# Performance work log

Measured on AMD Instinct MI355X. Metric: run time of the kernel, lower is better.

## Reference

```python
import jax, jax.numpy as jnp
import numpy as np

HIDDEN = 2048
N_HEADS = 32
N_KV = 8
HEAD_DIM = HIDDEN // N_HEADS  # 64
GROUP = N_HEADS // N_KV       # 4
FFN = 8192
EPS = 1e-5
ROPE_BASE = 500000.0
NEG = -1e9


def rms_norm(x, w, eps=EPS):
    var = jnp.mean(x * x, axis=-1, keepdims=True)
    return x * jax.lax.rsqrt(var + eps) * w


def rope_cos_sin(position_ids):
    # inv_freq: [head_dim//2]
    inv_freq = 1.0 / (ROPE_BASE ** (jnp.arange(0, HEAD_DIM, 2, dtype=jnp.float32) / HEAD_DIM))
    freqs = position_ids.astype(jnp.float32)[:, :, None] * inv_freq[None, None, :]  # [b,s,d/2]
    emb = jnp.concatenate([freqs, freqs], axis=-1)  # [b,s,d]
    return jnp.cos(emb), jnp.sin(emb)


def rotate_half(x):
    x1, x2 = jnp.split(x, 2, axis=-1)
    return jnp.concatenate([-x2, x1], axis=-1)


def setup_inputs() -> dict:
    key = jax.random.key(0)
    ks = jax.random.split(key, 12)
    b, s = 2, 1024
    scale_h = 1.0 / np.sqrt(HIDDEN)
    scale_f = 1.0 / np.sqrt(FFN)
    hidden_states = jax.random.normal(ks[0], (b, s, HIDDEN), jnp.float32)
    causal = jnp.where(jnp.tril(jnp.ones((s, s), bool)), 0.0, NEG).astype(jnp.float32)
    attention_mask = jnp.broadcast_to(causal[None, None], (b, 1, s, s))
    position_ids = jnp.broadcast_to(jnp.arange(s, dtype=jnp.int32)[None], (b, s))
    return {
        "hidden_states": hidden_states,
        "attention_mask": attention_mask,
        "wq": jax.random.normal(ks[1], (HIDDEN, N_HEADS * HEAD_DIM), jnp.float32) * scale_h,
        "wk": jax.random.normal(ks[2], (HIDDEN, N_KV * HEAD_DIM), jnp.float32) * scale_h,
        "wv": jax.random.normal(ks[3], (HIDDEN, N_KV * HEAD_DIM), jnp.float32) * scale_h,
        "wo": jax.random.normal(ks[4], (N_HEADS * HEAD_DIM, HIDDEN), jnp.float32) * scale_h,
        "norm1_w": jnp.ones((HIDDEN,), jnp.float32),
        "norm2_w": jnp.ones((HIDDEN,), jnp.float32),
        "w_gate": jax.random.normal(ks[5], (HIDDEN, FFN), jnp.float32) * scale_h,
        "w_up": jax.random.normal(ks[6], (HIDDEN, FFN), jnp.float32) * scale_h,
        "w_down": jax.random.normal(ks[7], (FFN, HIDDEN), jnp.float32) * scale_f,
        "position_ids": position_ids,
    }


def reference(hidden_states, attention_mask, wq, wk, wv, wo, norm1_w, norm2_w,
              w_gate, w_up, w_down, position_ids):
    b, s, _ = hidden_states.shape
    residual = hidden_states
    normed = rms_norm(hidden_states, norm1_w)

    q = (normed @ wq).reshape(b, s, N_HEADS, HEAD_DIM).transpose(0, 2, 1, 3)  # [b,H,s,d]
    k = (normed @ wk).reshape(b, s, N_KV, HEAD_DIM).transpose(0, 2, 1, 3)    # [b,G,s,d]
    v = (normed @ wv).reshape(b, s, N_KV, HEAD_DIM).transpose(0, 2, 1, 3)

    cos, sin = rope_cos_sin(position_ids)  # [b,s,d]
    cos, sin = cos[:, None], sin[:, None]  # unsqueeze head dim
    q = q * cos + rotate_half(q) * sin
    k = k * cos + rotate_half(k) * sin

    # repeat_kv: [b,G,s,d] -> [b,H,s,d]
    k = jnp.repeat(k, GROUP, axis=1)
    v = jnp.repeat(v, GROUP, axis=1)

    scores = jnp.einsum('bhqd,bhkd->bhqk', q, k)
    scores = scores + attention_mask  # mask added BEFORE scaling, as in source
    attn = jax.nn.softmax(scores / np.sqrt(HEAD_DIM), axis=-1)
    ctx = jnp.einsum('bhqk,bhkd->bhqd', attn, v)
    ctx = ctx.transpose(0, 2, 1, 3).reshape(b, s, N_HEADS * HEAD_DIM)
    attn_out = ctx @ wo

    normed_ff = rms_norm(attn_out + residual, norm2_w)
    ff = (jax.nn.silu(normed_ff @ w_gate) * (normed_ff @ w_up)) @ w_down
    return attn_out + ff
```

## Files before the change

### kernel.cpp

```cpp
#include <hip/hip_runtime.h>
#include <hip/hip_bf16.h>
#include <cstddef>
#include <cstdint>

#define T_TOK   2048
#define HID     2048
#define NHEADS  32
#define NKV     8
#define HDIM    64
#define FFN_DIM 8192
#define QKV_N   3072

typedef __hip_bfloat16 bf16;
typedef __attribute__((ext_vector_type(8))) short short8;
typedef __attribute__((ext_vector_type(4))) float f32x4;
typedef __attribute__((ext_vector_type(4))) unsigned short us4;

typedef __attribute__((address_space(1))) const void cg_void;
typedef __attribute__((address_space(3))) void lds_void;

__global__ __launch_bounds__(256) void cast_transpose(const float* __restrict__ in,
                                                      bf16* __restrict__ out,
                                                      int K, int N)
{
    __shared__ bf16 t[64][65];
    const int n0 = blockIdx.x * 64, k0 = blockIdx.y * 64;
    const int tn = threadIdx.x & 63, tk = threadIdx.x >> 6;
    #pragma unroll
    for (int kk = tk; kk < 64; kk += 4)
        t[kk][tn] = __float2bfloat16(in[(size_t)(k0 + kk) * N + n0 + tn]);
    __syncthreads();
    #pragma unroll
    for (int nn = tk; nn < 64; nn += 4)
        out[(size_t)(n0 + nn) * K + k0 + tn] = t[tn][nn];
}

__global__ __launch_bounds__(256) void rmsnorm_kernel(const float* __restrict__ x,
                                                      const float* __restrict__ w,
                                                      bf16* __restrict__ out)
{
    __shared__ float sm[4];
    const int row = blockIdx.x, tid = threadIdx.x;
    const float4* xr = (const float4*)(x + (size_t)row * HID);
    float4 a = xr[tid], b = xr[tid + 256];
    float ss = a.x*a.x + a.y*a.y + a.z*a.z + a.w*a.w
             + b.x*b.x + b.y*b.y + b.z*b.z + b.w*b.w;
    #pragma unroll
    for (int off = 32; off; off >>= 1) ss += __shfl_down(ss, off);
    if ((tid & 63) == 0) sm[tid >> 6] = ss;
    __syncthreads();
    float sc = rsqrtf((sm[0] + sm[1] + sm[2] + sm[3]) * (1.0f / HID) + 1e-5f);
    const float4* wr = (const float4*)w;
    float4 w0 = wr[tid], w1 = wr[tid + 256];
    bf16* o = out + (size_t)row * HID;
    o[tid*4+0] = __float2bfloat16(a.x * sc * w0.x);
    o[tid*4+1] = __float2bfloat16(a.y * sc * w0.y);
    o[tid*4+2] = __float2bfloat16(a.z * sc * w0.z);
    o[tid*4+3] = __float2bfloat16(a.w * sc * w0.w);
    o[1024+tid*4+0] = __float2bfloat16(b.x * sc * w1.x);
    o[1024+tid*4+1] = __float2bfloat16(b.y * sc * w1.y);
    o[1024+tid*4+2] = __float2bfloat16(b.z * sc * w1.z);
    o[1024+tid*4+3] = __float2bfloat16(b.w * sc * w1.w);
}

__global__ __launch_bounds__(256) void rmsnorm_add_kernel(const float* __restrict__ xa,
                                                          const float* __restrict__ xb,
                                                          const float* __restrict__ w,
                                                          bf16* __restrict__ out)
{
    __shared__ float sm[4];
    const int row = blockIdx.x, tid = threadIdx.x;
    const float4* ar = (const float4*)(xa + (size_t)row * HID);
    const float4* br = (const float4*)(xb + (size_t)row * HID);
    float4 a0 = ar[tid], a1 = ar[tid + 256];
    float4 b0 = br[tid], b1 = br[tid + 256];
    float4 s0, s1;
    s0.x = a0.x + b0.x; s0.y = a0.y + b0.y; s0.z = a0.z + b0.z; s0.w = a0.w + b0.w;
    s1.x = a1.x + b1.x; s1.y = a1.y + b1.y; s1.z = a1.z + b1.z; s1.w = a1.w + b1.w;
    float ss = s0.x*s0.x + s0.y*s0.y + s0.z*s0.z + s0.w*s0.w
             + s1.x*s1.x + s1.y*s1.y + s1.z*s1.z + s1.w*s1.w;
    #pragma unroll
    for (int off = 32; off; off >>= 1) ss += __shfl_down(ss, off);
    if ((tid & 63) == 0) sm[tid >> 6] = ss;
    __syncthreads();
    float sc = rsqrtf((sm[0] + sm[1] + sm[2] + sm[3]) * (1.0f / HID) + 1e-5f);
    const float4* wr = (const float4*)w;
    float4 w0 = wr[tid], w1 = wr[tid + 256];
    bf16* o = out + (size_t)row * HID;
    o[tid*4+0] = __float2bfloat16(s0.x * sc * w0.x);
    o[tid*4+1] = __float2bfloat16(s0.y * sc * w0.y);
    o[tid*4+2] = __float2bfloat16(s0.z * sc * w0.z);
    o[tid*4+3] = __float2bfloat16(s0.w * sc * w0.w);
    o[1024+tid*4+0] = __float2bfloat16(s1.x * sc * w1.x);
    o[1024+tid*4+1] = __float2bfloat16(s1.y * sc * w1.y);
    o[1024+tid*4+2] = __float2bfloat16(s1.z * sc * w1.z);
    o[1024+tid*4+3] = __float2bfloat16(s1.w * sc * w1.w);
}

template<int BN, int EPI>
__global__ __launch_bounds__(256) void mfma_gemm(
    const bf16* __restrict__ A, const bf16* __restrict__ Bt,
    float* __restrict__ Cf, bf16* __restrict__ Cb, const bf16* __restrict__ aux,
    int M, int N, int K, int ldc, int ldaux)
{
    constexpr int NFR = BN / 32;
    constexpr int BCH = BN / 32;
    __shared__ bf16 As[128 * 64];
    __shared__ bf16 Bs[BN * 64];
    const int tid = threadIdx.x;
    const int wv = tid >> 6, ln = tid & 63;
    const int wr = wv >> 1, wc = wv & 1;

    const int nwg = gridDim.x * gridDim.y;
    int orig = blockIdx.y * gridDim.x + blockIdx.x;
    int wg = (orig & 7) * (nwg >> 3) + (orig >> 3);
    const int bx = wg % gridDim.x, by = wg / gridDim.x;
    const size_t m0 = (size_t)by * 128;
    const size_t n0 = (size_t)bx * BN;

    const int lrow = ln >> 3;
    const int lk   = (ln & 7) ^ lrow;

    f32x4 acc[4][NFR] = {};

    const bf16* Abase = A  + (m0 + (size_t)(wv*4)*8 + lrow) * K + lk*8;
    const bf16* Bbase = Bt + (n0 + (size_t)(wv*BCH)*8 + lrow) * K + lk*8;
    bf16* AsW = As + wv*4*512;
    bf16* BsW = Bs + wv*BCH*512;

    for (int kt = 0; kt < K; kt += 64) {
        #pragma unroll
        for (int i = 0; i < 4; ++i)
            __builtin_amdgcn_global_load_lds((cg_void*)(Abase + (size_t)i*8*K + kt),
                                             (lds_void*)(AsW + i*512), 16, 0, 0);
        #pragma unroll
        for (int i = 0; i < BCH; ++i)
            __builtin_amdgcn_global_load_lds((cg_void*)(Bbase + (size_t)i*8*K + kt),
                                             (lds_void*)(BsW + i*512), 16, 0, 0);
        __syncthreads();
        #pragma unroll
        for (int ks = 0; ks < 2; ++ks) {
            short8 af[4], bfg[NFR];
            const int kbyte = ks*64 + (ln >> 4)*16;
            #pragma unroll
            for (int m = 0; m < 4; ++m) {
                int row = wr*64 + m*16 + (ln & 15);
                af[m] = *(const short8*)((const char*)As + row*128 + (kbyte ^ ((row & 7) << 4)));
            }
            #pragma unroll
            for (int n = 0; n < NFR; ++n) {
                int row = wc*(BN/2) + n*16 + (ln & 15);
                bfg[n] = *(const short8*)((const char*)Bs + row*128 + (kbyte ^ ((row & 7) << 4)));
            }
            #pragma unroll
            for (int m = 0; m < 4; ++m)
                #pragma unroll
                for (int n = 0; n < NFR; ++n)
                    acc[m][n] = __builtin_amdgcn_mfma_f32_16x16x32_bf16(af[m], bfg[n], acc[m][n], 0, 0, 0);
        }
        __syncthreads();
    }

    const int cj = ln & 15, rj = ln >> 4;
    #pragma unroll
    for (int m = 0; m < 4; ++m) {
        #pragma unroll
        for (int j = 0; j < 4; ++j) {
            size_t row = m0 + wr*64 + m*16 + rj*4 + j;
            #pragma unroll
            for (int n = 0; n < NFR; ++n) {
                int col = (int)n0 + wc*(BN/2) + n*16 + cj;
                float v = acc[m][n][j];
                size_t off = row * (size_t)ldc + col;
                if constexpr (EPI == 0) {
                    Cf[off] = v;
                } else if constexpr (EPI == 1) {
                    Cf[off] += v;
                } else if constexpr (EPI == 2) {
                    Cb[off] = __float2bfloat16(v / (1.0f + __expf(-v)));
                } else {
                    float g = __bfloat162float(aux[row * (size_t)ldaux + col]);
                    Cb[off] = __float2bfloat16(g * v);
                }
            }
        }
    }
}

__global__ __launch_bounds__(256) void rope_cast(const float* __restrict__ qkv,
                                                 const int* __restrict__ pos_ids,
                                                 bf16* __restrict__ Qp,
                                                 bf16* __restrict__ Kp)
{
    const int t = blockIdx.x, tid = threadIdx.x;
    const int b = t >> 10, s = t & 1023;
    const float pos = (float)pos_ids[t];
    const float* row = qkv + (size_t)t * QKV_N;

    {
        int idx = tid * 4;
        int hq = idx >> 5, j = idx & 31;
        float xa[4], xb[4];
        *(float4*)xa = *(const float4*)(row + hq*64 + j);
        *(float4*)xb = *(const float4*)(row + hq*64 + j + 32);
        us4 o1, o2;
        #pragma unroll
        for (int jj = 0; jj < 4; ++jj) {
            float inv = exp2f(-(float)(j + jj) * 0.5916115177913804f);
            float ang = pos * inv, c, sn;
            sincosf(ang, &sn, &c);
            o1[jj] = __bfloat16_as_ushort(__float2bfloat16(xa[jj]*c - xb[jj]*sn));
            o2[jj] = __bfloat16_as_ushort(__float2bfloat16(xb[jj]*c + xa[jj]*sn));
        }
        bf16* qd = Qp + ((size_t)(b*32 + hq)*1024 + s)*64;
        *(us4*)(qd + j)      = o1;
        *(us4*)(qd + j + 32) = o2;
    }
    {
        int hk = tid >> 5, j = tid & 31;
        float a = row[2048 + hk*64 + j];
        float bb = row[2048 + hk*64 + j + 32];
        float inv = exp2f(-(float)j * 0.5916115177913804f);
        float ang = pos * inv, c, sn;
        sincosf(ang, &sn, &c);
        bf16* kd = Kp + ((size_t)(b*8 + hk)*1024 + s)*64;
        kd[j]      = __float2bfloat16(a*c - bb*sn);
        kd[j + 32] = __float2bfloat16(bb*c + a*sn);
    }
}

__global__ __launch_bounds__(256) void vt_cast(const float* __restrict__ qkv,
                                               bf16* __restrict__ Vt)
{
    __shared__ bf16 tile[64][64];
    const int s0 = blockIdx.x * 64;
    const int sec = blockIdx.y;
    const int b = sec >> 3, hk = sec & 7;
    const int tid = threadIdx.x;
    const float* base = qkv + ((size_t)(b*1024 + s0)) * QKV_N + 2560 + hk*64;
    const int srow = tid >> 2, d0 = (tid & 3) * 16;
    #pragma unroll
    for (int q = 0; q < 4; ++q) {
        float va[4];
        *(float4*)va = *(const float4*)(base + (size_t)srow * QKV_N + d0 + q*4);
        #pragma unroll
        for (int cc = 0; cc < 4; ++cc)
            tile[d0 + q*4 + cc][srow] = __float2bfloat16(va[cc]);
    }
    __syncthreads();
    const int dr = tid >> 2, sc = (tid & 3) * 16;
    bf16* od = Vt + ((size_t)sec*64 + dr)*1024 + s0 + sc;
    *(short8*)od       = *(const short8*)&tile[dr][sc];
    *(short8*)(od + 8) = *(const short8*)&tile[dr][sc + 8];
}

__global__ __launch_bounds__(256) void attn_mfma(const bf16* __restrict__ Qp,
                                                 const bf16* __restrict__ Kp,
                                                 const bf16* __restrict__ Vt,
                                                 bf16* __restrict__ ctx)
{
    __shared__ bf16 Ks[128 * 64];
    __shared__ bf16 Vs[64 * 128];
    __shared__ bf16 Ps[4 * 32 * 128];
    const int tid = threadIdx.x;
    const int w = tid >> 6, ln = tid & 63;
    const int qt = blockIdx.x, h = blockIdx.y, b = blockIdx.z;
    const int hk = h >> 2;
    const int q0 = qt * 128;

    const bf16* qsec = Qp + ((size_t)(b*32 + h)*1024 + q0 + w*32)*64;
    const bf16* ksec = Kp + ((size_t)(b*8 + hk)*1024)*64;
    const bf16* vsec = Vt + ((size_t)(b*8 + hk))*64*1024;

    short8 qf[2][2];
    #pragma unroll
    for (int f = 0; f < 2; ++f)
        #pragma unroll
        for (int kc = 0; kc < 2; ++kc)
            qf[f][kc] = *(const short8*)(qsec + (size_t)(f*16 + (ln & 15))*64 + kc*32 + (ln >> 4)*8);

    f32x4 acc_o[2][4] = {};
    f32x4 m[2], l[2];
    #pragma unroll
    for (int f = 0; f < 2; ++f)
        #pragma unroll
        for (int j = 0; j < 4; ++j) { m[f][j] = -1e30f; l[f][j] = 0.0f; }

    const int lrow = ln >> 3;
    const int lkk  = (ln & 7) ^ lrow;
    char* PsW = (char*)Ps + w * 8192;

    const int ntiles = qt + 1;
    for (int kt = 0; kt < ntiles; ++kt) {
        const int kv0 = kt * 128;
        {
            const bf16* kbase = ksec + (size_t)(kv0 + w*32 + lrow)*64 + lkk*8;
            bf16* KsW = Ks + w*2048;
            #pragma unroll
            for (int i = 0; i < 4; ++i)
                __builtin_amdgcn_global_load_lds((cg_void*)(kbase + (size_t)i*8*64),
                                                 (lds_void*)(KsW + i*512), 16, 0, 0);
        }
        {
            bf16* VsW = Vs + w*2048;
            #pragma unroll
            for (int i = 0; i < 4; ++i) {
                int d = w*16 + i*4 + (ln >> 4);
                __builtin_amdgcn_global_load_lds(
                    (cg_void*)(vsec + (size_t)d*1024 + kv0 + (((ln & 15) ^ (d & 7))*8)),
                    (lds_void*)(VsW + i*512), 16, 0, 0);
            }
        }
        __syncthreads();

        f32x4 acc_s[2][8] = {};
        #pragma unroll
        for (int c = 0; c < 8; ++c) {
            int kvr = c*16 + (ln & 15);
            const char* krow = (const char*)Ks + kvr*128;
            short8 kf0 = *(const short8*)(krow + (((ln >> 4)*16)      ^ ((kvr & 7) << 4)));
            short8 kf1 = *(const short8*)(krow + ((64 + (ln >> 4)*16) ^ ((kvr & 7) << 4)));
            #pragma unroll
            for (int f = 0; f < 2; ++f) {
                acc_s[f][c] = __builtin_amdgcn_mfma_f32_16x16x32_bf16(qf[f][0], kf0, acc_s[f][c], 0, 0, 0);
                acc_s[f][c] = __builtin_amdgcn_mfma_f32_16x16x32_bf16(qf[f][1], kf1, acc_s[f][c], 0, 0, 0);
            }
        }

        const bool diag = (kt == qt);
        f32x4 vmax[2];
        #pragma unroll
        for (int f = 0; f < 2; ++f)
            #pragma unroll
            for (int j = 0; j < 4; ++j) vmax[f][j] = -1e30f;
        #pragma unroll
        for (int f = 0; f < 2; ++f) {
            #pragma unroll
            for (int c = 0; c < 8; ++c) {
                f32x4 t = acc_s[f][c] * 0.125f;
                if (diag) {
                    int kv = kv0 + c*16 + (ln & 15);
                    int qg = q0 + w*32 + f*16 + (ln >> 4)*4;
                    #pragma unroll
                    for (int j = 0; j < 4; ++j)
                        if (kv > qg + j) t[j] = -1e30f;
                }
                acc_s[f][c] = t;
                #pragma unroll
                for (int j = 0; j < 4; ++j) vmax[f][j] = fmaxf(vmax[f][j], t[j]);
            }
            #pragma unroll
            for (int mk = 1; mk <= 8; mk <<= 1)
                #pragma unroll
                for (int j = 0; j < 4; ++j)
                    vmax[f][j] = fmaxf(vmax[f][j], __shfl_xor(vmax[f][j], mk));
        }

        #pragma unroll
        for (int f = 0; f < 2; ++f) {
            f32x4 r;
            #pragma unroll
            for (int j = 0; j < 4; ++j) {
                float mn = fmaxf(m[f][j], vmax[f][j]);
                r[j] = __expf(m[f][j] - mn);
                m[f][j] = mn;
                l[f][j] *= r[j];
            }
            #pragma unroll
            for (int df = 0; df < 4; ++df)
                #pragma unroll
                for (int j = 0; j < 4; ++j) acc_o[f][df][j] *= r[j];
        }

        f32x4 rs[2] = {};
        #pragma unroll
        for (int f = 0; f < 2; ++f) {
            #pragma unroll
            for (int c = 0; c < 8; ++c) {
                #pragma unroll
                for (int j = 0; j < 4; ++j) {
                    float p = __expf(acc_s[f][c][j] - m[f][j]);
                    rs[f][j] += p;
                    int qloc = f*16 + (ln >> 4)*4 + j;
                    int kvb  = (c*16 + (ln & 15))*2;
                    *(bf16*)(PsW + qloc*256 + (kvb ^ ((qloc & 7) << 4))) = __float2bfloat16(p);
                }
            }
            #pragma unroll
            for (int mk = 1; mk <= 8; mk <<= 1)
                #pragma unroll
                for (int j = 0; j < 4; ++j)
                    rs[f][j] += __shfl_xor(rs[f][j], mk);
            #pragma unroll
            for (int j = 0; j < 4; ++j) l[f][j] += rs[f][j];
        }

        #pragma unroll
        for (int kc = 0; kc < 4; ++kc) {
            short8 pa[2];
            #pragma unroll
            for (int f = 0; f < 2; ++f) {
                int qloc = f*16 + (ln & 15);
                pa[f] = *(const short8*)(PsW + qloc*256 + ((kc*64 + (ln >> 4)*16) ^ ((qloc & 7) << 4)));
            }
            #pragma unroll
            for (int df = 0; df < 4; ++df) {
                int dl = df*16 + (ln & 15);
                short8 vfr = *(const short8*)((const char*)Vs + dl*256 + ((kc*64 + (ln >> 4)*16) ^ ((dl & 7) << 4)));
                #pragma unroll
                for (int f = 0; f < 2; ++f)
                    acc_o[f][df] = __builtin_amdgcn_mfma_f32_16x16x32_bf16(pa[f], vfr, acc_o[f][df], 0, 0, 0);
            }
        }
        __syncthreads();
    }

    #pragma unroll
    for (int f = 0; f < 2; ++f) {
        f32x4 inv;
        #pragma unroll
        for (int j = 0; j < 4; ++j) inv[j] = 1.0f / l[f][j];
        #pragma unroll
        for (int df = 0; df < 4; ++df) {
            #pragma unroll
            for (int j = 0; j < 4; ++j) {
                int q = q0 + w*32 + f*16 + (ln >> 4)*4 + j;
                int d = df*16 + (ln & 15);
                ctx[((size_t)b*1024 + q)*HID + h*64 + d] = __float2bfloat16(acc_o[f][df][j] * inv[j]);
            }
        }
    }
}

extern "C" void kernel_launch(void* const* d_in, const int* in_sizes, int n_in,
                              void* d_out, int out_size, void* d_ws, size_t ws_size,
                              hipStream_t stream)
{
    const float* hidden = (const float*)d_in[0];
    const float* wq = (const float*)d_in[2];
    const float* wk = (const float*)d_in[3];
    const float* wv = (const float*)d_in[4];
    const float* wo = (const float*)d_in[5];
    const float* n1 = (const float*)d_in[6];
    const float* n2 = (const float*)d_in[7];
    const float* wg = (const float*)d_in[8];
    const float* wu = (const float*)d_in[9];
    const float* wd = (const float*)d_in[10];
    const int*  pos = (const int*)d_in[11];
    float* out = (float*)d_out;
    char* ws = (char*)d_ws;

    bf16* wg_t   = (bf16*)(ws + 0);
    bf16* wu_t   = (bf16*)(ws + 33554432);
    bf16* wd_t   = (bf16*)(ws + 67108864);
    bf16* wqkv_t = (bf16*)(ws + 100663296);
    bf16* wo_t   = (bf16*)(ws + 113246208);
    bf16* normed = (bf16*)(ws + 121634816);
    float* qkv   = (float*)(ws + 130023424);
    bf16* ctx    = (bf16*)(ws + 155189248);
    bf16* hb     = (bf16*)(ws + 130023424);
    bf16* gbh    = (bf16*)(ws + 163577856);
    bf16* Qp     = (bf16*)(ws + 121634816);
    bf16* Kp     = (bf16*)(ws + 163577856);
    bf16* Vt     = (bf16*)(ws + 165675008);

    cast_transpose<<<dim3(32, 32), 256, 0, stream>>>(wq, wqkv_t, 2048, 2048);
    cast_transpose<<<dim3(8, 32),  256, 0, stream>>>(wk, wqkv_t + 4194304, 2048, 512);
    cast_transpose<<<dim3(8, 32),  256, 0, stream>>>(wv, wqkv_t + 5242880, 2048, 512);
    cast_transpose<<<dim3(32, 32), 256, 0, stream>>>(wo, wo_t, 2048, 2048);
    cast_transpose<<<dim3(128, 32),256, 0, stream>>>(wg, wg_t, 2048, 8192);
    cast_transpose<<<dim3(128, 32),256, 0, stream>>>(wu, wu_t, 2048, 8192);
    cast_transpose<<<dim3(32, 128),256, 0, stream>>>(wd, wd_t, 8192, 2048);

    rmsnorm_kernel<<<T_TOK, 256, 0, stream>>>(hidden, n1, normed);
    mfma_gemm<64,0><<<dim3(QKV_N/64, T_TOK/128), 256, 0, stream>>>(
        normed, wqkv_t, qkv, nullptr, nullptr, T_TOK, QKV_N, HID, QKV_N, 0);
    rope_cast<<<T_TOK, 256, 0, stream>>>(qkv, pos, Qp, Kp);
    vt_cast<<<dim3(16, 16), 256, 0, stream>>>(qkv, Vt);
    attn_mfma<<<dim3(8, NHEADS, 2), 256, 0, stream>>>(Qp, Kp, Vt, ctx);
    mfma_gemm<64,0><<<dim3(HID/64, T_TOK/128), 256, 0, stream>>>(
        ctx, wo_t, out, nullptr, nullptr, T_TOK, HID, HID, HID, 0);
    rmsnorm_add_kernel<<<T_TOK, 256, 0, stream>>>(out, hidden, n2, normed);
    for (int hh = 0; hh < 2; ++hh) {
        mfma_gemm<64,2><<<dim3(4096/64, T_TOK/128), 256, 0, stream>>>(
            normed, wg_t + (size_t)hh*4096*2048, nullptr, gbh, nullptr,
            T_TOK, 4096, HID, 4096, 0);
        mfma_gemm<64,3><<<dim3(4096/64, T_TOK/128), 256, 0, stream>>>(
            normed, wu_t + (size_t)hh*4096*2048, nullptr, hb + (size_t)hh*4096, gbh,
            T_TOK, 4096, HID, 8192, 4096);
    }
    mfma_gemm<64,1><<<dim3(HID/64, T_TOK/128), 256, 0, stream>>>(
        hb, wd_t, out, nullptr, nullptr, T_TOK, HID, FFN_DIM, HID, 0);
}
```

Measured before the change: 595.6 us.

## Fuse gate and up GEMMs via interleaved weights, split-K down projection

Gate and up weight columns are interleaved in 32-column groups during the cast, so one GEMM with BN=128 computes both and applies silu(g)*u in the epilogue. This removes the bf16 gate intermediate and its re-read, and replaces four launches with one. The down projection is split into two K halves across blockIdx.z, each accumulating into the output with atomic adds. That doubles the grid for better occupancy, at the cost of atomic traffic and non-deterministic summation order.

```diff
diff --git a/kernel.cpp b/kernel.cpp
--- a/kernel.cpp
+++ b/kernel.cpp
@@ -33,6 +33,25 @@
     #pragma unroll
     for (int nn = tk; nn < 64; nn += 4)
         out[(size_t)(n0 + nn) * K + k0 + tn] = t[tn][nn];
+}
+
+__global__ __launch_bounds__(256) void cast_ilv(const float* __restrict__ in,
+                                                bf16* __restrict__ out,
+                                                int N, int is_up)
+{
+    __shared__ bf16 t[64][65];
+    const int n0 = blockIdx.x * 64, k0 = blockIdx.y * 64;
+    const int tn = threadIdx.x & 63, tk = threadIdx.x >> 6;
+    #pragma unroll
+    for (int kk = tk; kk < 64; kk += 4)
+        t[kk][tn] = __float2bfloat16(in[(size_t)(k0 + kk) * N + n0 + tn]);
+    __syncthreads();
+    #pragma unroll
+    for (int nn = tk; nn < 64; nn += 4) {
+        int n = n0 + nn;
+        int r = ((n >> 5) << 6) + (is_up << 5) + (n & 31);
+        out[(size_t)r * HID + k0 + tn] = t[tn][nn];
+    }
 }
 
 __global__ __launch_bounds__(256) void rmsnorm_kernel(const float* __restrict__ x,
@@ -98,10 +117,10 @@
 }
 
 template<int BN, int EPI>
-__global__ __launch_bounds__(256) void mfma_gemm(
+__device__ __forceinline__ void gemm_body(
     const bf16* __restrict__ A, const bf16* __restrict__ Bt,
-    float* __restrict__ Cf, bf16* __restrict__ Cb, const bf16* __restrict__ aux,
-    int M, int N, int K, int ldc, int ldaux)
+    float* __restrict__ Cf, bf16* __restrict__ Cb,
+    int lda, int kbeg, int klen, int ldc, int bx, int by)
 {
     constexpr int NFR = BN / 32;
     constexpr int BCH = BN / 32;
@@ -110,81 +129,118 @@
     const int tid = threadIdx.x;
     const int wv = tid >> 6, ln = tid & 63;
     const int wr = wv >> 1, wc = wv & 1;
-
+    const size_t m0 = (size_t)by * 128;
+    const size_t n0 = (size_t)bx * BN;
+
+    const int lrow = ln >> 3;
+    const int lk   = (ln & 7) ^ lrow;
+
+    f32x4 acc[4][NFR] = {};
+
+    const bf16* Abase = A  + (m0 + (size_t)wv*32 + lrow) * lda + kbeg + lk*8;
+    const bf16* Bbase = Bt + (n0 + (size_t)wv*BCH*8 + lrow) * lda + kbeg + lk*8;
+    bf16* AsW = As + wv*4*512;
+    bf16* BsW = Bs + wv*BCH*512;
+
+    for (int kt = 0; kt < klen; kt += 64) {
+        #pragma unroll
+        for (int i = 0; i < 4; ++i)
+            __builtin_amdgcn_global_load_lds((cg_void*)(Abase + (size_t)i*8*lda + kt),
+                                             (lds_void*)(AsW + i*512), 16, 0, 0);
+        #pragma unroll
+        for (int i = 0; i < BCH; ++i)
+            __builtin_amdgcn_global_load_lds((cg_void*)(Bbase + (size_t)i*8*lda + kt),
+                                             (lds_void*)(BsW + i*512), 16, 0, 0);
+        __syncthreads();
+        #pragma unroll
+        for (int ks = 0; ks < 2; ++ks) {
+            short8 af[4], bfg[NFR];
+            const int kbyte = ks*64 + (ln >> 4)*16;
+            #pragma unroll
+            for (int m = 0; m < 4; ++m) {
+                int row = wr*64 + m*16 + (ln & 15);
+                af[m] = *(const short8*)((const char*)As + row*128 + (kbyte ^ ((row & 7) << 4)));
+            }
+            #pragma unroll
+            for (int n = 0; n < NFR; ++n) {
+                int row = wc*(BN/2) + n*16 + (ln & 15);
+                bfg[n] = *(const short8*)((const char*)Bs + row*128 + (kbyte ^ ((row & 7) << 4)));
+            }
+            #pragma unroll
+            for (int m = 0; m < 4; ++m)
+                #pragma unroll
+                for (int n = 0; n < NFR; ++n)
+                    acc[m][n] = __builtin_amdgcn_mfma_f32_16x16x32_bf16(af[m], bfg[n], acc[m][n], 0, 0, 0);
+        }
+        __syncthreads();
+    }
+
+    const int cj = ln & 15, rj = ln >> 4;
+    if constexpr (EPI == 4) {
+        #pragma unroll
+        for (int m = 0; m < 4; ++m) {
+            #pragma unroll
+            for (int j = 0; j < 4; ++j) {
+                size_t row = m0 + wr*64 + m*16 + rj*4 + j;
+                #pragma unroll
+                for (int n = 0; n < 2; ++n) {
+                    int col = ((int)(n0 >> 6) + wc) * 32 + n*16 + cj;
+                    float g = acc[m][n][j];
+                    float u = acc[m][n+2][j];
+                    Cb[row * (size_t)ldc + col] =
+                        __float2bfloat16(g / (1.0f + __expf(-g)) * u);
+                }
+            }
+        }
+    } else {
+        #pragma unroll
+        for (int m = 0; m < 4; ++m) {
+            #pragma unroll
+            for (int j = 0; j < 4; ++j) {
+                size_t row = m0 + wr*64 + m*16 + rj*4 + j;
+                #pragma unroll
+                for (int n = 0; n < NFR; ++n) {
+                    int col = (int)n0 + wc*(BN/2) + n*16 + cj;
+                    float v = acc[m][n][j];
+                    size_t off = row * (size_t)ldc + col;
+                    if constexpr (EPI == 0) Cf[off] = v;
+                    else if constexpr (EPI == 5) unsafeAtomicAdd(&Cf[off], v);
+                }
+            }
+        }
+    }
+}
+
+__device__ __forceinline__ void swz(int& bx, int& by) {
     const int nwg = gridDim.x * gridDim.y;
     int orig = blockIdx.y * gridDim.x + blockIdx.x;
     int wg = (orig & 7) * (nwg >> 3) + (orig >> 3);
-    const int bx = wg % gridDim.x, by = wg / gridDim.x;
-    const size_t m0 = (size_t)by * 128;
-    const size_t n0 = (size_t)bx * BN;
-
-    const int lrow = ln >> 3;
-    const int lk   = (ln & 7) ^ lrow;
-
-    f32x4 acc[4][NFR] = {};
-
-    const bf16* Abase = A  + (m0 + (size_t)(wv*4)*8 + lrow) * K + lk*8;
-    const bf16* Bbase = Bt + (n0 + (size_t)(wv*BCH)*8 + lrow) * K + lk*8;
-    bf16* AsW = As + wv*4*512;
-    bf16* BsW = Bs + wv*BCH*512;
-
-    for (int kt = 0; kt < K; kt += 64) {
-        #pragma unroll
-        for (int i = 0; i < 4; ++i)
-            __builtin_amdgcn_global_load_lds((cg_void*)(Abase + (size_t)i*8*K + kt),
-                                             (lds_void*)(AsW + i*512), 16, 0, 0);
-        #pragma unroll
-        for (int i = 0; i < BCH; ++i)
-            __builtin_amdgcn_global_load_lds((cg_void*)(Bbase + (size_t)i*8*K + kt),
-                                             (lds_void*)(BsW + i*512), 16, 0, 0);
-        __syncthreads();
-        #pragma unroll
-        for (int ks = 0; ks < 2; ++ks) {
-            short8 af[4], bfg[NFR];
-            const int kbyte = ks*64 + (ln >> 4)*16;
-            #pragma unroll
-            for (int m = 0; m < 4; ++m) {
-                int row = wr*64 + m*16 + (ln & 15);
-                af[m] = *(const short8*)((const char*)As + row*128 + (kbyte ^ ((row & 7) << 4)));
-            }
-            #pragma unroll
-            for (int n = 0; n < NFR; ++n) {
-                int row = wc*(BN/2) + n*16 + (ln & 15);
-                bfg[n] = *(const short8*)((const char*)Bs + row*128 + (kbyte ^ ((row & 7) << 4)));
-            }
-            #pragma unroll
-            for (int m = 0; m < 4; ++m)
-                #pragma unroll
-                for (int n = 0; n < NFR; ++n)
-                    acc[m][n] = __builtin_amdgcn_mfma_f32_16x16x32_bf16(af[m], bfg[n], acc[m][n], 0, 0, 0);
-        }
-        __syncthreads();
-    }
-
-    const int cj = ln & 15, rj = ln >> 4;
-    #pragma unroll
-    for (int m = 0; m < 4; ++m) {
-        #pragma unroll
-        for (int j = 0; j < 4; ++j) {
-            size_t row = m0 + wr*64 + m*16 + rj*4 + j;
-            #pragma unroll
-            for (int n = 0; n < NFR; ++n) {
-                int col = (int)n0 + wc*(BN/2) + n*16 + cj;
-                float v = acc[m][n][j];
-                size_t off = row * (size_t)ldc + col;
-                if constexpr (EPI == 0) {
-                    Cf[off] = v;
-                } else if constexpr (EPI == 1) {
-                    Cf[off] += v;
-                } else if constexpr (EPI == 2) {
-                    Cb[off] = __float2bfloat16(v / (1.0f + __expf(-v)));
-                } else {
-                    float g = __bfloat162float(aux[row * (size_t)ldaux + col]);
-                    Cb[off] = __float2bfloat16(g * v);
-                }
-            }
-        }
-    }
+    bx = wg % gridDim.x; by = wg / gridDim.x;
+}
+
+__global__ __launch_bounds__(256) void g_qkv(const bf16* __restrict__ A,
+                                             const bf16* __restrict__ Bt,
+                                             float* __restrict__ C) {
+    int bx, by; swz(bx, by);
+    gemm_body<64,0>(A, Bt, C, nullptr, HID, 0, HID, QKV_N, bx, by);
+}
+__global__ __launch_bounds__(256) void g_wo(const bf16* __restrict__ A,
+                                            const bf16* __restrict__ Bt,
+                                            float* __restrict__ C) {
+    int bx, by; swz(bx, by);
+    gemm_body<64,0>(A, Bt, C, nullptr, HID, 0, HID, HID, bx, by);
+}
+__global__ __launch_bounds__(256) void g_gateup(const bf16* __restrict__ A,
+                                                const bf16* __restrict__ Bt,
+                                                bf16* __restrict__ C) {
+    int bx, by; swz(bx, by);
+    gemm_body<128,4>(A, Bt, nullptr, C, HID, 0, HID, FFN_DIM, bx, by);
+}
+__global__ __launch_bounds__(256) void g_down(const bf16* __restrict__ A,
+                                              const bf16* __restrict__ Bt,
+                                              float* __restrict__ C) {
+    int bx, by; swz(bx, by);
+    gemm_body<64,5>(A, Bt, C, nullptr, FFN_DIM, blockIdx.z * 4096, 4096, HID, bx, by);
 }
 
 __global__ __launch_bounds__(256) void rope_cast(const float* __restrict__ qkv,
@@ -450,8 +506,7 @@
     float* out = (float*)d_out;
     char* ws = (char*)d_ws;
 
-    bf16* wg_t   = (bf16*)(ws + 0);
-    bf16* wu_t   = (bf16*)(ws + 33554432);
+    bf16* wgu_t  = (bf16*)(ws + 0);
     bf16* wd_t   = (bf16*)(ws + 67108864);
     bf16* wqkv_t = (bf16*)(ws + 100663296);
     bf16* wo_t   = (bf16*)(ws + 113246208);
@@ -459,7 +514,6 @@
     float* qkv   = (float*)(ws + 130023424);
     bf16* ctx    = (bf16*)(ws + 155189248);
     bf16* hb     = (bf16*)(ws + 130023424);
-    bf16* gbh    = (bf16*)(ws + 163577856);
     bf16* Qp     = (bf16*)(ws + 121634816);
     bf16* Kp     = (bf16*)(ws + 163577856);
     bf16* Vt     = (bf16*)(ws + 165675008);
@@ -468,27 +522,17 @@
     cast_transpose<<<dim3(8, 32),  256, 0, stream>>>(wk, wqkv_t + 4194304, 2048, 512);
     cast_transpose<<<dim3(8, 32),  256, 0, stream>>>(wv, wqkv_t + 5242880, 2048, 512);
     cast_transpose<<<dim3(32, 32), 256, 0, stream>>>(wo, wo_t, 2048, 2048);
-    cast_transpose<<<dim3(128, 32),256, 0, stream>>>(wg, wg_t, 2048, 8192);
-    cast_transpose<<<dim3(128, 32),256, 0, stream>>>(wu, wu_t, 2048, 8192);
+    cast_ilv<<<dim3(128, 32), 256, 0, stream>>>(wg, wgu_t, FFN_DIM, 0);
+    cast_ilv<<<dim3(128, 32), 256, 0, stream>>>(wu, wgu_t, FFN_DIM, 1);
     cast_transpose<<<dim3(32, 128),256, 0, stream>>>(wd, wd_t, 8192, 2048);
 
     rmsnorm_kernel<<<T_TOK, 256, 0, stream>>>(hidden, n1, normed);
-    mfma_gemm<64,0><<<dim3(QKV_N/64, T_TOK/128), 256, 0, stream>>>(
-        normed, wqkv_t, qkv, nullptr, nullptr, T_TOK, QKV_N, HID, QKV_N, 0);
+    g_qkv<<<dim3(QKV_N/64, T_TOK/128), 256, 0, stream>>>(normed, wqkv_t, qkv);
     rope_cast<<<T_TOK, 256, 0, stream>>>(qkv, pos, Qp, Kp);
     vt_cast<<<dim3(16, 16), 256, 0, stream>>>(qkv, Vt);
     attn_mfma<<<dim3(8, NHEADS, 2), 256, 0, stream>>>(Qp, Kp, Vt, ctx);
-    mfma_gemm<64,0><<<dim3(HID/64, T_TOK/128), 256, 0, stream>>>(
-        ctx, wo_t, out, nullptr, nullptr, T_TOK, HID, HID, HID, 0);
+    g_wo<<<dim3(HID/64, T_TOK/128), 256, 0, stream>>>(ctx, wo_t, out);
     rmsnorm_add_kernel<<<T_TOK, 256, 0, stream>>>(out, hidden, n2, normed);
-    for (int hh = 0; hh < 2; ++hh) {
-        mfma_gemm<64,2><<<dim3(4096/64, T_TOK/128), 256, 0, stream>>>(
-            normed, wg_t + (size_t)hh*4096*2048, nullptr, gbh, nullptr,
-            T_TOK, 4096, HID, 4096, 0);
-        mfma_gemm<64,3><<<dim3(4096/64, T_TOK/128), 256, 0, stream>>>(
-            normed, wu_t + (size_t)hh*4096*2048, nullptr, hb + (size_t)hh*4096, gbh,
-            T_TOK, 4096, HID, 8192, 4096);
-    }
-    mfma_gemm<64,1><<<dim3(HID/64, T_TOK/128), 256, 0, stream>>>(
-        hb, wd_t, out, nullptr, nullptr, T_TOK, HID, FFN_DIM, HID, 0);
-}
+    g_gateup<<<dim3(16384/128, T_TOK/128), 256, 0, stream>>>(normed, wgu_t, hb);
+    g_down<<<dim3(HID/64, T_TOK/128, 2), 256, 0, stream>>>(hb, wd_t, out);
+}
```

After: 532.4 us. 1.12x faster.
